# Performance work log

Measured on AMD Instinct MI355X. Metric: run time of the kernel, lower is better.

Reference implementation:

```python
import jax, jax.numpy as jnp
import numpy as np

B = 256
D = 2048          # in_channels (shared latent dim)
S = 8             # n_subjects
OUT = 1000        # sum of 7 Schaefer network head widths [150,148,132,136,76,122,236]


def setup_inputs() -> dict:
    key = jax.random.key(0)
    k1, k2, k3, k4 = jax.random.split(key, 4)
    x = jax.random.normal(k1, (B, D), dtype=jnp.float32)
    subject_ids = jax.random.randint(k2, (B,), 0, S, dtype=jnp.int64)
    scale = 1.0 / np.sqrt(D)  # matches normal_(0, 1/in_channels**0.5)
    # Concatenated per-head weights: equivalent to 7 heads of shapes
    # (S, D, n_k) concatenated along the output axis (n_k sums to OUT).
    W = jax.random.normal(k3, (S, D, OUT), dtype=jnp.float32) * scale
    b = jax.random.normal(k4, (S, OUT), dtype=jnp.float32) * scale
    return {"x": x, "subject_ids": subject_ids, "W": W, "b": b}


def reference(x, subject_ids, W, b):
    # Per-sample weight gather (B, D, OUT) followed by batched matmul,
    # exactly mirroring torch: w = weights[subject_ids]; einsum('bd,bdo->bo').
    w = W[subject_ids]                      # (B, D, OUT) gathered copy
    out = jnp.einsum('bd,bdo->bo', x, w)    # (B, OUT)
    out = out + b[subject_ids]              # per-subject bias
    return out
```

## Files before the change

kernel.cpp:

```cpp
#include <hip/hip_runtime.h>
#include <stdint.h>

#define Bn   256
#define Dn   2048
#define Sn   8
#define ON   1000

#define ROWS 64
#define OT   64
#define KC   256
#define NDC  (Dn / KC)
#define NCH  (KC / 32)
#define NIT  (KC / 32)
#define LDK  (KC + 8)

typedef short v8s __attribute__((ext_vector_type(8)));
typedef float v4f __attribute__((ext_vector_type(4)));

static __device__ __forceinline__ short f2bf(float f) {
    union { float f; uint32_t u; } v; v.f = f;
    uint32_t u = v.u;
    u += 0x7FFFu + ((u >> 16) & 1u);
    return (short)(u >> 16);
}

__global__ __launch_bounds__(256) void main_kernel(const float* __restrict__ x,
                                                   const int* __restrict__ sid,
                                                   const float* __restrict__ W,
                                                   float* __restrict__ part) {
    __shared__ unsigned short Ash[ROWS * LDK];
    __shared__ unsigned short Bsh[OT * LDK];
    __shared__ unsigned long long bmask[4];
    __shared__ int rows_l[ROWS];

    const int oc = blockIdx.x;
    const int dc = blockIdx.y;
    const int s  = blockIdx.z;
    const int o0 = oc * OT;
    const int d0 = dc * KC;
    const int t  = threadIdx.x;
    const int lane = t & 63;
    const int wave = t >> 6;

    const int mysid = sid[t];
    const bool match = (mysid == s);
    const unsigned long long m = __ballot(match);
    if (lane == 0) bmask[wave] = m;
    if (t < ROWS) rows_l[t] = -1;
    __syncthreads();
    if (match) {
        int pos = __popcll(m & ((1ull << lane) - 1ull));
        for (int w = 0; w < wave; ++w) pos += __popcll(bmask[w]);
        if (pos < ROWS) rows_l[pos] = t;
    }
    __syncthreads();

    const int arow = t >> 2;
    const int ag   = t & 3;
    const int xrow = rows_l[arow];
    const float* xp = (xrow >= 0) ? (x + (size_t)xrow * Dn + d0 + ag * 8) : x;
    const int aoff0 = arow * LDK + ag * 8;

    int og = o0 + lane; if (og > ON - 1) og = ON - 1;
    const float* wp = W + (size_t)s * Dn * ON + (size_t)(d0 + wave * 8) * ON + og;
    const int boff0 = lane * LDK + wave * 8;

    float4 fa[2][2];
    float  fb[2][8];
#pragma unroll
    for (int c = 0; c < 2; ++c) {
#pragma unroll
        for (int j = 0; j < 8; j++) fb[c][j] = wp[(size_t)(c * 32 + j) * ON];
        fa[c][0] = *(const float4*)(xp + c * 32);
        fa[c][1] = *(const float4*)(xp + c * 32 + 4);
    }

#pragma unroll
    for (int c = 0; c < NCH; ++c) {
        const int sl = c & 1;
        v8s av;
        av[0] = f2bf(fa[sl][0].x); av[1] = f2bf(fa[sl][0].y);
        av[2] = f2bf(fa[sl][0].z); av[3] = f2bf(fa[sl][0].w);
        av[4] = f2bf(fa[sl][1].x); av[5] = f2bf(fa[sl][1].y);
        av[6] = f2bf(fa[sl][1].z); av[7] = f2bf(fa[sl][1].w);
        *(v8s*)&Ash[aoff0 + c * 32] = av;

        v8s bv;
#pragma unroll
        for (int j = 0; j < 8; j++) bv[j] = f2bf(fb[sl][j]);
        *(v8s*)&Bsh[boff0 + c * 32] = bv;

        if (c + 2 < NCH) {
#pragma unroll
            for (int j = 0; j < 8; j++) fb[sl][j] = wp[(size_t)((c + 2) * 32 + j) * ON];
            fa[sl][0] = *(const float4*)(xp + (c + 2) * 32);
            fa[sl][1] = *(const float4*)(xp + (c + 2) * 32 + 4);
        }
    }

    __syncthreads();

    const int lo16 = lane & 15;
    const int quad = lane >> 4;
    const int ar   = wave * 16 + lo16;

    v4f acc[4];
#pragma unroll
    for (int i = 0; i < 4; i++) acc[i] = (v4f){0.f, 0.f, 0.f, 0.f};

#pragma unroll
    for (int it = 0; it < NIT; ++it) {
        const v8s af = *(const v8s*)&Ash[ar * LDK + it * 32 + quad * 8];
#pragma unroll
        for (int nt = 0; nt < 4; nt++) {
            const v8s bf = *(const v8s*)&Bsh[(nt * 16 + lo16) * LDK + it * 32 + quad * 8];
            acc[nt] = __builtin_amdgcn_mfma_f32_16x16x32_bf16(af, bf, acc[nt], 0, 0, 0);
        }
    }

    float* pp = part + (size_t)dc * Bn * ON;
    const int er0 = wave * 16 + quad * 4;
#pragma unroll
    for (int nt = 0; nt < 4; nt++) {
        const int o = o0 + nt * 16 + lo16;
        if (o < ON) {
#pragma unroll
            for (int r = 0; r < 4; r++) {
                const int bi = rows_l[er0 + r];
                if (bi >= 0) pp[(size_t)bi * ON + o] = acc[nt][r];
            }
        }
    }
}

__global__ __launch_bounds__(256) void reduce_kernel(const int* __restrict__ sid,
                                                     const float* __restrict__ bias,
                                                     const float* __restrict__ part,
                                                     float* __restrict__ out) {
    const int b = blockIdx.x;
    const int s = sid[b];
    const int o = threadIdx.x * 4;
    if (o < ON) {
        float4 v = *(const float4*)(bias + (size_t)s * ON + o);
#pragma unroll
        for (int d = 0; d < NDC; d++) {
            const float4 p = *(const float4*)(part + ((size_t)d * Bn + b) * ON + o);
            v.x += p.x; v.y += p.y; v.z += p.z; v.w += p.w;
        }
        *(float4*)(out + (size_t)b * ON + o) = v;
    }
}

extern "C" void kernel_launch(void* const* d_in, const int* in_sizes, int n_in,
                              void* d_out, int out_size, void* d_ws, size_t ws_size,
                              hipStream_t stream) {
    const float* x    = (const float*)d_in[0];
    const int*   sid  = (const int*)d_in[1];
    const float* W    = (const float*)d_in[2];
    const float* bias = (const float*)d_in[3];
    float*       out  = (float*)d_out;
    float*       part = (float*)d_ws;

    main_kernel<<<dim3(16, NDC, Sn), dim3(256), 0, stream>>>(x, sid, W, part);
    reduce_kernel<<<dim3(Bn), dim3(256), 0, stream>>>(sid, bias, part, out);
}
```

Baseline: 110.9 us.

## Pre-gather and pre-convert x per subject to bf16, load A fragments directly

Adds a gather kernel that packs the rows of x for each subject into a contiguous bf16 buffer in the workspace. The main kernel then loads its MFMA A fragments straight from global memory into registers, which drops the A shared-memory tile, the repeated fp32-to-bf16 conversion in each block, and the scattered row loads. The main kernel also gets a launch-bounds occupancy hint. The cost is an extra kernel launch and an extra workspace write and read.

```diff
diff --git a/kernel.cpp b/kernel.cpp
--- a/kernel.cpp
+++ b/kernel.cpp
@@ -24,11 +24,44 @@
     return (short)(u >> 16);
 }
 
-__global__ __launch_bounds__(256) void main_kernel(const float* __restrict__ x,
-                                                   const int* __restrict__ sid,
-                                                   const float* __restrict__ W,
-                                                   float* __restrict__ part) {
-    __shared__ unsigned short Ash[ROWS * LDK];
+__global__ __launch_bounds__(256) void gather_kernel(const float* __restrict__ x,
+                                                     const int* __restrict__ sid,
+                                                     unsigned short* __restrict__ xg) {
+    __shared__ unsigned long long bmask[4];
+    __shared__ int brow;
+    const int r = blockIdx.x;
+    const int s = blockIdx.y;
+    const int t = threadIdx.x;
+    const int lane = t & 63;
+    const int wave = t >> 6;
+
+    const bool match = (sid[t] == s);
+    const unsigned long long m = __ballot(match);
+    if (lane == 0) bmask[wave] = m;
+    if (t == 0) brow = -1;
+    __syncthreads();
+    if (match) {
+        int pos = __popcll(m & ((1ull << lane) - 1ull));
+        for (int w = 0; w < wave; ++w) pos += __popcll(bmask[w]);
+        if (pos == r) brow = t;
+    }
+    __syncthreads();
+
+    const int b = brow;
+    v8s v = (v8s){0, 0, 0, 0, 0, 0, 0, 0};
+    if (b >= 0) {
+        const float4 f0 = *(const float4*)(x + (size_t)b * Dn + t * 8);
+        const float4 f1 = *(const float4*)(x + (size_t)b * Dn + t * 8 + 4);
+        v[0] = f2bf(f0.x); v[1] = f2bf(f0.y); v[2] = f2bf(f0.z); v[3] = f2bf(f0.w);
+        v[4] = f2bf(f1.x); v[5] = f2bf(f1.y); v[6] = f2bf(f1.z); v[7] = f2bf(f1.w);
+    }
+    *(v8s*)(xg + ((size_t)s * ROWS + r) * Dn + t * 8) = v;
+}
+
+__global__ __launch_bounds__(256, 4) void main_kernel(const unsigned short* __restrict__ xg,
+                                                      const int* __restrict__ sid,
+                                                      const float* __restrict__ W,
+                                                      float* __restrict__ part) {
     __shared__ unsigned short Bsh[OT * LDK];
     __shared__ unsigned long long bmask[4];
     __shared__ int rows_l[ROWS];
@@ -55,54 +88,38 @@
     }
     __syncthreads();
 
-    const int arow = t >> 2;
-    const int ag   = t & 3;
-    const int xrow = rows_l[arow];
-    const float* xp = (xrow >= 0) ? (x + (size_t)xrow * Dn + d0 + ag * 8) : x;
-    const int aoff0 = arow * LDK + ag * 8;
-
     int og = o0 + lane; if (og > ON - 1) og = ON - 1;
     const float* wp = W + (size_t)s * Dn * ON + (size_t)(d0 + wave * 8) * ON + og;
     const int boff0 = lane * LDK + wave * 8;
 
-    float4 fa[2][2];
-    float  fb[2][8];
+    float fb[2][8];
 #pragma unroll
-    for (int c = 0; c < 2; ++c) {
+    for (int c = 0; c < 2; ++c)
 #pragma unroll
-        for (int j = 0; j < 8; j++) fb[c][j] = wp[(size_t)(c * 32 + j) * ON];
-        fa[c][0] = *(const float4*)(xp + c * 32);
-        fa[c][1] = *(const float4*)(xp + c * 32 + 4);
-    }
+        for (int j = 0; j < 8; ++j) fb[c][j] = wp[(size_t)(c * 32 + j) * ON];
+
+    const int lo16 = lane & 15;
+    const int quad = lane >> 4;
+    const int ar   = wave * 16 + lo16;
+    const unsigned short* xr = xg + ((size_t)s * ROWS + ar) * Dn + d0 + quad * 8;
+    v8s af[NIT];
+#pragma unroll
+    for (int it = 0; it < NIT; ++it) af[it] = *(const v8s*)(xr + it * 32);
 
 #pragma unroll
     for (int c = 0; c < NCH; ++c) {
         const int sl = c & 1;
-        v8s av;
-        av[0] = f2bf(fa[sl][0].x); av[1] = f2bf(fa[sl][0].y);
-        av[2] = f2bf(fa[sl][0].z); av[3] = f2bf(fa[sl][0].w);
-        av[4] = f2bf(fa[sl][1].x); av[5] = f2bf(fa[sl][1].y);
-        av[6] = f2bf(fa[sl][1].z); av[7] = f2bf(fa[sl][1].w);
-        *(v8s*)&Ash[aoff0 + c * 32] = av;
-
         v8s bv;
 #pragma unroll
-        for (int j = 0; j < 8; j++) bv[j] = f2bf(fb[sl][j]);
+        for (int j = 0; j < 8; ++j) bv[j] = f2bf(fb[sl][j]);
         *(v8s*)&Bsh[boff0 + c * 32] = bv;
-
         if (c + 2 < NCH) {
 #pragma unroll
-            for (int j = 0; j < 8; j++) fb[sl][j] = wp[(size_t)((c + 2) * 32 + j) * ON];
-            fa[sl][0] = *(const float4*)(xp + (c + 2) * 32);
-            fa[sl][1] = *(const float4*)(xp + (c + 2) * 32 + 4);
+            for (int j = 0; j < 8; ++j) fb[sl][j] = wp[(size_t)((c + 2) * 32 + j) * ON];
         }
     }
 
     __syncthreads();
-
-    const int lo16 = lane & 15;
-    const int quad = lane >> 4;
-    const int ar   = wave * 16 + lo16;
 
     v4f acc[4];
 #pragma unroll
@@ -110,11 +127,10 @@
 
 #pragma unroll
     for (int it = 0; it < NIT; ++it) {
-        const v8s af = *(const v8s*)&Ash[ar * LDK + it * 32 + quad * 8];
 #pragma unroll
         for (int nt = 0; nt < 4; nt++) {
             const v8s bf = *(const v8s*)&Bsh[(nt * 16 + lo16) * LDK + it * 32 + quad * 8];
-            acc[nt] = __builtin_amdgcn_mfma_f32_16x16x32_bf16(af, bf, acc[nt], 0, 0, 0);
+            acc[nt] = __builtin_amdgcn_mfma_f32_16x16x32_bf16(af[it], bf, acc[nt], 0, 0, 0);
         }
     }
 
@@ -160,7 +176,9 @@
     const float* bias = (const float*)d_in[3];
     float*       out  = (float*)d_out;
     float*       part = (float*)d_ws;
+    unsigned short* xg = (unsigned short*)((char*)d_ws + (size_t)NDC * Bn * ON * sizeof(float));
 
-    main_kernel<<<dim3(16, NDC, Sn), dim3(256), 0, stream>>>(x, sid, W, part);
+    gather_kernel<<<dim3(ROWS, Sn), dim3(256), 0, stream>>>(x, sid, xg);
+    main_kernel<<<dim3(16, NDC, Sn), dim3(256), 0, stream>>>(xg, sid, W, part);
     reduce_kernel<<<dim3(Bn), dim3(256), 0, stream>>>(sid, bias, part, out);
 }
```

Measured after the change: 110.8 us. About the same (-0.1%).

## Drop split-K and reduce kernel; loop full K with double-buffered weight tiles

Applied to the files above, without the earlier changes.

Replaces the split-K grid and its separate reduction kernel with a single kernel in which each block walks the whole 2048-long K dimension for a 32-column output tile. Weight tiles are prefetched into registers and double-buffered in shared memory, and x is converted straight from global memory into MFMA fragments. Bias is added in the epilogue. This removes the partial-sum round trip through the workspace and the second launch. The cost is fewer blocks (256 instead of 1024) and a longer serial K loop per block, so latency hiding depends on the register prefetch.

```diff
diff --git a/kernel.cpp b/kernel.cpp
--- a/kernel.cpp
+++ b/kernel.cpp
@@ -7,11 +7,9 @@
 #define ON   1000
 
 #define ROWS 64
-#define OT   64
+#define OT   32
 #define KC   256
-#define NDC  (Dn / KC)
-#define NCH  (KC / 32)
-#define NIT  (KC / 32)
+#define NKT  (Dn / KC)
 #define LDK  (KC + 8)
 
 typedef short v8s __attribute__((ext_vector_type(8)));
@@ -27,23 +25,20 @@
 __global__ __launch_bounds__(256) void main_kernel(const float* __restrict__ x,
                                                    const int* __restrict__ sid,
                                                    const float* __restrict__ W,
-                                                   float* __restrict__ part) {
-    __shared__ unsigned short Ash[ROWS * LDK];
-    __shared__ unsigned short Bsh[OT * LDK];
+                                                   const float* __restrict__ bias,
+                                                   float* __restrict__ out) {
+    __shared__ unsigned short Bsh[2][OT * LDK];
     __shared__ unsigned long long bmask[4];
     __shared__ int rows_l[ROWS];
 
     const int oc = blockIdx.x;
-    const int dc = blockIdx.y;
-    const int s  = blockIdx.z;
+    const int s  = blockIdx.y;
     const int o0 = oc * OT;
-    const int d0 = dc * KC;
     const int t  = threadIdx.x;
     const int lane = t & 63;
     const int wave = t >> 6;
 
-    const int mysid = sid[t];
-    const bool match = (mysid == s);
+    const bool match = (sid[t] == s);
     const unsigned long long m = __ballot(match);
     if (lane == 0) bmask[wave] = m;
     if (t < ROWS) rows_l[t] = -1;
@@ -55,99 +50,109 @@
     }
     __syncthreads();
 
-    const int arow = t >> 2;
-    const int ag   = t & 3;
-    const int xrow = rows_l[arow];
-    const float* xp = (xrow >= 0) ? (x + (size_t)xrow * Dn + d0 + ag * 8) : x;
-    const int aoff0 = arow * LDK + ag * 8;
-
-    int og = o0 + lane; if (og > ON - 1) og = ON - 1;
-    const float* wp = W + (size_t)s * Dn * ON + (size_t)(d0 + wave * 8) * ON + og;
-    const int boff0 = lane * LDK + wave * 8;
-
-    float4 fa[2][2];
-    float  fb[2][8];
-#pragma unroll
-    for (int c = 0; c < 2; ++c) {
-#pragma unroll
-        for (int j = 0; j < 8; j++) fb[c][j] = wp[(size_t)(c * 32 + j) * ON];
-        fa[c][0] = *(const float4*)(xp + c * 32);
-        fa[c][1] = *(const float4*)(xp + c * 32 + 4);
-    }
-
-#pragma unroll
-    for (int c = 0; c < NCH; ++c) {
-        const int sl = c & 1;
-        v8s av;
-        av[0] = f2bf(fa[sl][0].x); av[1] = f2bf(fa[sl][0].y);
-        av[2] = f2bf(fa[sl][0].z); av[3] = f2bf(fa[sl][0].w);
-        av[4] = f2bf(fa[sl][1].x); av[5] = f2bf(fa[sl][1].y);
-        av[6] = f2bf(fa[sl][1].z); av[7] = f2bf(fa[sl][1].w);
-        *(v8s*)&Ash[aoff0 + c * 32] = av;
-
-        v8s bv;
-#pragma unroll
-        for (int j = 0; j < 8; j++) bv[j] = f2bf(fb[sl][j]);
-        *(v8s*)&Bsh[boff0 + c * 32] = bv;
-
-        if (c + 2 < NCH) {
-#pragma unroll
-            for (int j = 0; j < 8; j++) fb[sl][j] = wp[(size_t)((c + 2) * 32 + j) * ON];
-            fa[sl][0] = *(const float4*)(xp + (c + 2) * 32);
-            fa[sl][1] = *(const float4*)(xp + (c + 2) * 32 + 4);
-        }
-    }
-
-    __syncthreads();
+    int og = o0 + (t & 31); if (og > ON - 1) og = ON - 1;
+    const int kr = t >> 5;
+    const float* wp = W + (size_t)s * Dn * ON + (size_t)(kr * 32) * ON + og;
+    const int boff = (t & 31) * LDK + kr * 32;
 
     const int lo16 = lane & 15;
     const int quad = lane >> 4;
     const int ar   = wave * 16 + lo16;
+    const int xrow = rows_l[ar];
+    const float* xp = (xrow >= 0 ? x + (size_t)xrow * Dn : x) + quad * 8;
+    const bool wactive = (rows_l[wave * 16] >= 0);
 
-    v4f acc[4];
+    float fbr0[32], fbr1[32];
 #pragma unroll
-    for (int i = 0; i < 4; i++) acc[i] = (v4f){0.f, 0.f, 0.f, 0.f};
+    for (int j = 0; j < 32; ++j) fbr0[j] = wp[(size_t)j * ON];
+#pragma unroll
+    for (int j = 0; j < 32; ++j) fbr1[j] = wp[((size_t)KC + j) * ON];
 
 #pragma unroll
-    for (int it = 0; it < NIT; ++it) {
-        const v8s af = *(const v8s*)&Ash[ar * LDK + it * 32 + quad * 8];
+    for (int g = 0; g < 4; ++g) {
+        v8s bv;
 #pragma unroll
-        for (int nt = 0; nt < 4; nt++) {
-            const v8s bf = *(const v8s*)&Bsh[(nt * 16 + lo16) * LDK + it * 32 + quad * 8];
-            acc[nt] = __builtin_amdgcn_mfma_f32_16x16x32_bf16(af, bf, acc[nt], 0, 0, 0);
-        }
+        for (int j = 0; j < 8; ++j) bv[j] = f2bf(fbr0[g * 8 + j]);
+        *(v8s*)&Bsh[0][boff + g * 8] = bv;
+    }
+    asm volatile("s_waitcnt lgkmcnt(0)" ::: "memory");
+    __builtin_amdgcn_s_barrier();
+    asm volatile("" ::: "memory");
+
+    v4f acc[2];
+    acc[0] = (v4f){0.f, 0.f, 0.f, 0.f};
+    acc[1] = (v4f){0.f, 0.f, 0.f, 0.f};
+
+#define COMPUTE_TILE(KT, BUF)                                                        \
+    if (wactive) {                                                                   \
+        _Pragma("unroll")                                                            \
+        for (int it = 0; it < 8; ++it) {                                             \
+            const float4 f0 = *(const float4*)(xp + (size_t)(KT) * KC + it * 32);    \
+            const float4 f1 = *(const float4*)(xp + (size_t)(KT) * KC + it * 32 + 4);\
+            v8s af;                                                                  \
+            af[0] = f2bf(f0.x); af[1] = f2bf(f0.y);                                  \
+            af[2] = f2bf(f0.z); af[3] = f2bf(f0.w);                                  \
+            af[4] = f2bf(f1.x); af[5] = f2bf(f1.y);                                  \
+            af[6] = f2bf(f1.z); af[7] = f2bf(f1.w);                                  \
+            _Pragma("unroll")                                                        \
+            for (int nt = 0; nt < 2; ++nt) {                                         \
+                const v8s bf = *(const v8s*)&Bsh[BUF][(nt * 16 + lo16) * LDK +       \
+                                                      it * 32 + quad * 8];           \
+                acc[nt] = __builtin_amdgcn_mfma_f32_16x16x32_bf16(af, bf, acc[nt],   \
+                                                                  0, 0, 0);          \
+            }                                                                        \
+        }                                                                            \
     }
 
-    float* pp = part + (size_t)dc * Bn * ON;
-    const int er0 = wave * 16 + quad * 4;
+#define CVT_TILE(FBR, BUF)                                                           \
+    {                                                                                \
+        _Pragma("unroll")                                                            \
+        for (int g = 0; g < 4; ++g) {                                                \
+            v8s bv;                                                                  \
+            _Pragma("unroll")                                                        \
+            for (int j = 0; j < 8; ++j) bv[j] = f2bf(FBR[g * 8 + j]);                \
+            *(v8s*)&Bsh[BUF][boff + g * 8] = bv;                                     \
+        }                                                                            \
+        asm volatile("s_waitcnt lgkmcnt(0)" ::: "memory");                           \
+        __builtin_amdgcn_s_barrier();                                                \
+        asm volatile("" ::: "memory");                                               \
+    }
+
+#define ISSUE_TILE(FBR, KT)                                                          \
+    {                                                                                \
+        _Pragma("unroll")                                                            \
+        for (int j = 0; j < 32; ++j) FBR[j] = wp[((size_t)(KT) * KC + j) * ON];      \
+    }
+
+#pragma unroll 1
+    for (int kt = 0; kt < NKT; kt += 2) {
+        if (kt + 2 < NKT) ISSUE_TILE(fbr0, kt + 2)
+        COMPUTE_TILE(kt, 0)
+        CVT_TILE(fbr1, 1)
+
+        if (kt + 3 < NKT) ISSUE_TILE(fbr1, kt + 3)
+        COMPUTE_TILE(kt + 1, 1)
+        if (kt + 2 < NKT) CVT_TILE(fbr0, 0)
+    }
+
+#undef COMPUTE_TILE
+#undef CVT_TILE
+#undef ISSUE_TILE
+
+    if (wactive) {
+        const int er0 = wave * 16 + quad * 4;
 #pragma unroll
-    for (int nt = 0; nt < 4; nt++) {
-        const int o = o0 + nt * 16 + lo16;
-        if (o < ON) {
+        for (int nt = 0; nt < 2; ++nt) {
+            const int o = o0 + nt * 16 + lo16;
+            if (o < ON) {
+                const float bv = bias[(size_t)s * ON + o];
 #pragma unroll
-            for (int r = 0; r < 4; r++) {
-                const int bi = rows_l[er0 + r];
-                if (bi >= 0) pp[(size_t)bi * ON + o] = acc[nt][r];
+                for (int r = 0; r < 4; ++r) {
+                    const int bi = rows_l[er0 + r];
+                    if (bi >= 0) out[(size_t)bi * ON + o] = acc[nt][r] + bv;
+                }
             }
         }
-    }
-}
-
-__global__ __launch_bounds__(256) void reduce_kernel(const int* __restrict__ sid,
-                                                     const float* __restrict__ bias,
-                                                     const float* __restrict__ part,
-                                                     float* __restrict__ out) {
-    const int b = blockIdx.x;
-    const int s = sid[b];
-    const int o = threadIdx.x * 4;
-    if (o < ON) {
-        float4 v = *(const float4*)(bias + (size_t)s * ON + o);
-#pragma unroll
-        for (int d = 0; d < NDC; d++) {
-            const float4 p = *(const float4*)(part + ((size_t)d * Bn + b) * ON + o);
-            v.x += p.x; v.y += p.y; v.z += p.z; v.w += p.w;
-        }
-        *(float4*)(out + (size_t)b * ON + o) = v;
     }
 }
 
@@ -159,8 +164,7 @@
     const float* W    = (const float*)d_in[2];
     const float* bias = (const float*)d_in[3];
     float*       out  = (float*)d_out;
-    float*       part = (float*)d_ws;
+    (void)d_ws; (void)ws_size;
 
-    main_kernel<<<dim3(16, NDC, Sn), dim3(256), 0, stream>>>(x, sid, W, part);
-    reduce_kernel<<<dim3(Bn), dim3(256), 0, stream>>>(sid, bias, part, out);
+    main_kernel<<<dim3(32, Sn), dim3(256), 0, stream>>>(x, sid, W, bias, out);
 }
```

Measured after the change: 140.8 us. 26.9% more time.

## Loop multiple K tiles per block, load A directly into registers, skip empty waves

Applied to the files above, without the earlier changes.

Each block now covers a quarter of the K dimension (512) by looping over two 256-wide tiles, instead of one block per 256-wide chunk. This cuts the grid and the partial-sum workspace from 8 slices to 4, so the reduce kernel reads less. The x operand is loaded straight from global memory into MFMA registers, removing the A shared-memory tile and its staging. Waves whose 16 rows hold no matching samples skip the MFMA work and the stores. The W loads are still prefetched across tiles, but with fewer blocks there may be less parallelism to hide memory latency, and the hand-written barriers add a sync between tiles.

```diff
diff --git a/kernel.cpp b/kernel.cpp
--- a/kernel.cpp
+++ b/kernel.cpp
@@ -8,10 +8,11 @@
 
 #define ROWS 64
 #define OT   64
+#define NDC  4
+#define KB   (Dn / NDC)
 #define KC   256
-#define NDC  (Dn / KC)
+#define NTL  (KB / KC)
 #define NCH  (KC / 32)
-#define NIT  (KC / 32)
 #define LDK  (KC + 8)
 
 typedef short v8s __attribute__((ext_vector_type(8)));
@@ -28,22 +29,20 @@
                                                    const int* __restrict__ sid,
                                                    const float* __restrict__ W,
                                                    float* __restrict__ part) {
-    __shared__ unsigned short Ash[ROWS * LDK];
     __shared__ unsigned short Bsh[OT * LDK];
     __shared__ unsigned long long bmask[4];
     __shared__ int rows_l[ROWS];
 
     const int oc = blockIdx.x;
-    const int dc = blockIdx.y;
+    const int kc = blockIdx.y;
     const int s  = blockIdx.z;
     const int o0 = oc * OT;
-    const int d0 = dc * KC;
+    const int d0 = kc * KB;
     const int t  = threadIdx.x;
     const int lane = t & 63;
     const int wave = t >> 6;
 
-    const int mysid = sid[t];
-    const bool match = (mysid == s);
+    const bool match = (sid[t] == s);
     const unsigned long long m = __ballot(match);
     if (lane == 0) bmask[wave] = m;
     if (t < ROWS) rows_l[t] = -1;
@@ -55,79 +54,84 @@
     }
     __syncthreads();
 
-    const int arow = t >> 2;
-    const int ag   = t & 3;
-    const int xrow = rows_l[arow];
-    const float* xp = (xrow >= 0) ? (x + (size_t)xrow * Dn + d0 + ag * 8) : x;
-    const int aoff0 = arow * LDK + ag * 8;
-
     int og = o0 + lane; if (og > ON - 1) og = ON - 1;
     const float* wp = W + (size_t)s * Dn * ON + (size_t)(d0 + wave * 8) * ON + og;
-    const int boff0 = lane * LDK + wave * 8;
-
-    float4 fa[2][2];
-    float  fb[2][8];
-#pragma unroll
-    for (int c = 0; c < 2; ++c) {
-#pragma unroll
-        for (int j = 0; j < 8; j++) fb[c][j] = wp[(size_t)(c * 32 + j) * ON];
-        fa[c][0] = *(const float4*)(xp + c * 32);
-        fa[c][1] = *(const float4*)(xp + c * 32 + 4);
-    }
-
-#pragma unroll
-    for (int c = 0; c < NCH; ++c) {
-        const int sl = c & 1;
-        v8s av;
-        av[0] = f2bf(fa[sl][0].x); av[1] = f2bf(fa[sl][0].y);
-        av[2] = f2bf(fa[sl][0].z); av[3] = f2bf(fa[sl][0].w);
-        av[4] = f2bf(fa[sl][1].x); av[5] = f2bf(fa[sl][1].y);
-        av[6] = f2bf(fa[sl][1].z); av[7] = f2bf(fa[sl][1].w);
-        *(v8s*)&Ash[aoff0 + c * 32] = av;
-
-        v8s bv;
-#pragma unroll
-        for (int j = 0; j < 8; j++) bv[j] = f2bf(fb[sl][j]);
-        *(v8s*)&Bsh[boff0 + c * 32] = bv;
-
-        if (c + 2 < NCH) {
-#pragma unroll
-            for (int j = 0; j < 8; j++) fb[sl][j] = wp[(size_t)((c + 2) * 32 + j) * ON];
-            fa[sl][0] = *(const float4*)(xp + (c + 2) * 32);
-            fa[sl][1] = *(const float4*)(xp + (c + 2) * 32 + 4);
-        }
-    }
-
-    __syncthreads();
+    const int boff = lane * LDK + wave * 8;
 
     const int lo16 = lane & 15;
     const int quad = lane >> 4;
     const int ar   = wave * 16 + lo16;
+    const int xrow = rows_l[ar];
+    const float* xp = (xrow >= 0 ? x + (size_t)xrow * Dn : x) + d0 + quad * 8;
+    const bool wactive = (rows_l[wave * 16] >= 0);
 
     v4f acc[4];
 #pragma unroll
     for (int i = 0; i < 4; i++) acc[i] = (v4f){0.f, 0.f, 0.f, 0.f};
 
+    float fb[2][8];
 #pragma unroll
-    for (int it = 0; it < NIT; ++it) {
-        const v8s af = *(const v8s*)&Ash[ar * LDK + it * 32 + quad * 8];
+    for (int c = 0; c < 2; ++c)
 #pragma unroll
-        for (int nt = 0; nt < 4; nt++) {
-            const v8s bf = *(const v8s*)&Bsh[(nt * 16 + lo16) * LDK + it * 32 + quad * 8];
-            acc[nt] = __builtin_amdgcn_mfma_f32_16x16x32_bf16(af, bf, acc[nt], 0, 0, 0);
+        for (int j = 0; j < 8; ++j) fb[c][j] = wp[(size_t)(c * 32 + j) * ON];
+
+#pragma unroll
+    for (int kt = 0; kt < NTL; ++kt) {
+#pragma unroll
+        for (int c = 0; c < NCH; ++c) {
+            const int sl = c & 1;
+            v8s bv;
+#pragma unroll
+            for (int j = 0; j < 8; ++j) bv[j] = f2bf(fb[sl][j]);
+            *(v8s*)&Bsh[boff + c * 32] = bv;
+            const int gi = kt * NCH + c + 2;
+            if (gi < NTL * NCH) {
+#pragma unroll
+                for (int j = 0; j < 8; ++j) fb[sl][j] = wp[((size_t)gi * 32 + j) * ON];
+            }
+        }
+        asm volatile("s_waitcnt lgkmcnt(0)" ::: "memory");
+        __builtin_amdgcn_s_barrier();
+        asm volatile("" ::: "memory");
+
+        if (wactive) {
+#pragma unroll
+            for (int it = 0; it < 8; ++it) {
+                const float4 f0 = *(const float4*)(xp + kt * KC + it * 32);
+                const float4 f1 = *(const float4*)(xp + kt * KC + it * 32 + 4);
+                v8s af;
+                af[0] = f2bf(f0.x); af[1] = f2bf(f0.y);
+                af[2] = f2bf(f0.z); af[3] = f2bf(f0.w);
+                af[4] = f2bf(f1.x); af[5] = f2bf(f1.y);
+                af[6] = f2bf(f1.z); af[7] = f2bf(f1.w);
+#pragma unroll
+                for (int nt = 0; nt < 4; ++nt) {
+                    const v8s bf = *(const v8s*)&Bsh[(nt * 16 + lo16) * LDK +
+                                                     it * 32 + quad * 8];
+                    acc[nt] = __builtin_amdgcn_mfma_f32_16x16x32_bf16(af, bf, acc[nt],
+                                                                      0, 0, 0);
+                }
+            }
+        }
+        if (kt + 1 < NTL) {
+            asm volatile("s_waitcnt lgkmcnt(0)" ::: "memory");
+            __builtin_amdgcn_s_barrier();
+            asm volatile("" ::: "memory");
         }
     }
 
-    float* pp = part + (size_t)dc * Bn * ON;
-    const int er0 = wave * 16 + quad * 4;
+    if (wactive) {
+        float* pp = part + (size_t)kc * Bn * ON;
+        const int er0 = wave * 16 + quad * 4;
 #pragma unroll
-    for (int nt = 0; nt < 4; nt++) {
-        const int o = o0 + nt * 16 + lo16;
-        if (o < ON) {
+        for (int nt = 0; nt < 4; ++nt) {
+            const int o = o0 + nt * 16 + lo16;
+            if (o < ON) {
 #pragma unroll
-            for (int r = 0; r < 4; r++) {
-                const int bi = rows_l[er0 + r];
-                if (bi >= 0) pp[(size_t)bi * ON + o] = acc[nt][r];
+                for (int r = 0; r < 4; ++r) {
+                    const int bi = rows_l[er0 + r];
+                    if (bi >= 0) pp[(size_t)bi * ON + o] = acc[nt][r];
+                }
             }
         }
     }
```

Measured after the change: 113.5 us. 2.3% more time.
